# Kernel optimization log

Hardware: AMD Instinct MI355X
Metric: run time of the kernel (lower is better)

## Reference

```python
import jax, jax.numpy as jnp
import numpy as np

D_MODEL = 1024
NUM_HEAD = 16
HEAD_DIM = D_MODEL // NUM_HEAD
D_OUT = 1024
B, S = 2, 2048


def setup_inputs() -> dict:
    key = jax.random.key(0)
    ks = jax.random.split(key, 11)
    s = 0.02
    return {
        "Q": jax.random.normal(ks[0], (B, S, D_MODEL), jnp.float32),
        "K": jax.random.normal(ks[1], (B, S, D_MODEL), jnp.float32),
        "V": jax.random.normal(ks[2], (B, S, D_MODEL), jnp.float32),
        "Wq": jax.random.normal(ks[3], (D_MODEL, D_MODEL), jnp.float32) * s,
        "bq": jnp.zeros((D_MODEL,), jnp.float32),
        "Wk": jax.random.normal(ks[4], (D_MODEL, D_MODEL), jnp.float32) * s,
        "bk": jnp.zeros((D_MODEL,), jnp.float32),
        "Wv": jax.random.normal(ks[5], (D_MODEL, D_MODEL), jnp.float32) * s,
        "bv": jnp.zeros((D_MODEL,), jnp.float32),
        "Wo": jax.random.normal(ks[6], (D_MODEL, D_OUT), jnp.float32) * s,
        "bo": jnp.zeros((D_OUT,), jnp.float32),
    }


def reference(Q, K, V, Wq, bq, Wk, bk, Wv, bv, Wo, bo):
    T = jnp.asarray(HEAD_DIM, Q.dtype) ** 0.5
    b = Q.shape[0]
    q = (Q @ Wq + bq) / T                      # [B,S,D]
    k = K @ Wk + bk
    v = V @ Wv + bv
    q = q.reshape(b, -1, NUM_HEAD, HEAD_DIM)   # [B,S,H,d]
    k = k.reshape(b, -1, NUM_HEAD, HEAD_DIM)
    v = v.reshape(b, -1, NUM_HEAD, HEAD_DIM)
    scores = jnp.einsum("bqhd,bkhd->bhqk", q, k)
    attn = jax.nn.softmax(scores, axis=-1)
    out = jnp.einsum("bhqk,bkhd->bqhd", attn, v).reshape(b, -1, D_MODEL)
    return out @ Wo + bo
```

## Files before the change

kernel.cpp:

```cpp
#include <hip/hip_runtime.h>
#include <cstdint>
#include <cstddef>

#define D_MODEL 1024
#define HD 64
#define NH 16
#define SEQ 2048
#define NB 2

typedef __attribute__((ext_vector_type(8))) short bf8;
typedef __attribute__((ext_vector_type(8))) unsigned short us8;
typedef __attribute__((ext_vector_type(4))) unsigned short us4;
typedef __attribute__((ext_vector_type(4))) float f4;

__device__ __forceinline__ float bf2f(unsigned short u) {
  union { unsigned int i; float f; } c; c.i = ((unsigned int)u) << 16; return c.f;
}
__device__ __forceinline__ unsigned short f2bf(float x) {
  union { float f; unsigned int i; } c; c.f = x;
  unsigned int r = (c.i + 0x7FFFu + ((c.i >> 16) & 1u)) >> 16;
  return (unsigned short)r;
}
__device__ __forceinline__ unsigned int pkbf(float lo, float hi) {
  unsigned int r;
  asm("v_cvt_pk_bf16_f32 %0, %1, %2" : "=v"(r) : "v"(lo), "v"(hi));
  return r;
}
__device__ __forceinline__ float ex2(float x) {
  float r;
  asm("v_exp_f32 %0, %1" : "=v"(r) : "v"(x));
  return r;
}
__device__ __forceinline__ f4 mfma16(bf8 a, bf8 b, f4 c) {
  return __builtin_amdgcn_mfma_f32_16x16x32_bf16(a, b, c, 0, 0, 0);
}
__device__ __forceinline__ void gl16(const unsigned short* g, unsigned short* l) {
  __builtin_amdgcn_global_load_lds(
      (const __attribute__((address_space(1))) unsigned int*)g,
      (__attribute__((address_space(3))) unsigned int*)l, 16, 0, 0);
}

#define QSCALE (0.125f * 1.44269504088896f)

__global__ __launch_bounds__(256) void prep_weights(
    const float* __restrict__ Wq, const float* __restrict__ Wk,
    const float* __restrict__ Wv, const float* __restrict__ Wo,
    unsigned short* __restrict__ wthi) {
  int bid = blockIdx.x;
  int mat = bid >> 10, rem = bid & 1023;
  int kt = (rem >> 5) * 32, nt = (rem & 31) * 32;
  const float* W = (mat == 0) ? Wq : (mat == 1) ? Wk : (mat == 2) ? Wv : Wo;
  unsigned short* oh = wthi + ((size_t)mat << 20);
  __shared__ float ls[32][33];
  int i = threadIdx.x >> 5;
  int jj = threadIdx.x & 31;
#pragma unroll
  for (int ii = 0; ii < 4; ++ii) {
    int r = i + ii * 8;
    ls[r][jj] = W[(size_t)(kt + r) * D_MODEL + nt + jj];
  }
  __syncthreads();
#pragma unroll
  for (int ii = 0; ii < 4; ++ii) {
    int r = i + ii * 8;
    float v = ls[jj][r];
    if (mat == 0) v *= QSCALE;
    oh[(size_t)(nt + r) * D_MODEL + kt + jj] = f2bf(v);
  }
}

__global__ __launch_bounds__(256, 3) void proj_gemm(
    const float* __restrict__ Qin, const float* __restrict__ Kin,
    const float* __restrict__ Vin, const unsigned short* __restrict__ wth,
    const float* __restrict__ b0, const float* __restrict__ b1,
    const float* __restrict__ b2,
    unsigned short* __restrict__ qh, unsigned short* __restrict__ kh,
    unsigned short* __restrict__ vt) {
  int wid = (blockIdx.x & 7) * 96 + (blockIdx.x >> 3);
  int z = wid >> 8, rem = wid & 255, bm = rem >> 3, bn = rem & 7;

  const float* A = (z == 0) ? Qin : (z == 1) ? Kin : Vin;
  const unsigned short* Bh = wth + ((size_t)z << 20);
  const float* bias = (z == 0) ? b0 : (z == 1) ? b1 : b2;
  float bsc = (z == 0) ? QSCALE : 1.0f;

  int tid = threadIdx.x, lane = tid & 63, w = tid >> 6;
  int wr = w >> 1, wc = w & 1, l16 = lane & 15, l4 = lane >> 4;

  __shared__ unsigned short As[2][128 * 32];
  __shared__ unsigned short Bsh[2][128 * 32];

  const float* Ab = A + (size_t)(bm * 128) * D_MODEL;
  const unsigned short* Bhb = Bh + (size_t)(bn * 128) * D_MODEL;

  int r0 = tid >> 2, g0 = tid & 3;
  int r1 = (256 + tid) >> 2, g1 = tid & 3;
  int s0 = (r0 ^ (r0 >> 2)) & 3, s1 = (r1 ^ (r1 >> 2)) & 3;
  size_t so0 = (size_t)r0 * D_MODEL + ((g0 ^ s0) * 8);
  size_t so1 = (size_t)r1 * D_MODEL + ((g1 ^ s1) * 8);
  int ld0 = (w * 64) * 8;
  int ld1 = (256 + w * 64) * 8;

  int rr = tid >> 2, c8 = (tid & 3) * 8;
  int adst[2];
#pragma unroll
  for (int p = 0; p < 2; ++p) {
    int row = p * 64 + rr;
    int sw = (row ^ (row >> 2)) & 3;
    adst[p] = row * 32 + (((tid & 3) ^ sw)) * 8;
  }

  int offA[4], offB[4];
#pragma unroll
  for (int m = 0; m < 4; ++m) {
    int row = wr * 64 + m * 16 + l16;
    int sw = (row ^ (row >> 2)) & 3;
    offA[m] = row * 32 + ((l4 ^ sw)) * 8;
  }
#pragma unroll
  for (int n = 0; n < 4; ++n) {
    int row = wc * 64 + n * 16 + l16;
    int sw = (row ^ (row >> 2)) & 3;
    offB[n] = row * 32 + ((l4 ^ sw)) * 8;
  }

  f4 acc[4][4];
  const f4 zf = {0.f, 0.f, 0.f, 0.f};
#pragma unroll
  for (int m = 0; m < 4; ++m)
#pragma unroll
    for (int n = 0; n < 4; ++n) acc[m][n] = zf;

  {
    float4 x[2][2];
#pragma unroll
    for (int p = 0; p < 2; ++p) {
      const float* src = Ab + (size_t)(p * 64 + rr) * D_MODEL + c8;
      x[p][0] = *reinterpret_cast<const float4*>(src);
      x[p][1] = *reinterpret_cast<const float4*>(src + 4);
    }
    gl16(Bhb + so0, &Bsh[0][ld0]);
    gl16(Bhb + so1, &Bsh[0][ld1]);
#pragma unroll
    for (int p = 0; p < 2; ++p) {
      union { us8 v; unsigned u[4]; } hv;
      hv.u[0] = pkbf(x[p][0].x, x[p][0].y); hv.u[1] = pkbf(x[p][0].z, x[p][0].w);
      hv.u[2] = pkbf(x[p][1].x, x[p][1].y); hv.u[3] = pkbf(x[p][1].z, x[p][1].w);
      *reinterpret_cast<us8*>(&As[0][adst[p]]) = hv.v;
    }
  }
  __syncthreads();

  int cur = 0;
  for (int i = 0; i < 32; ++i) {
    float4 nx[2][2];
    if (i < 31) {
      int ktn = (i + 1) * 32;
#pragma unroll
      for (int p = 0; p < 2; ++p) {
        const float* src = Ab + (size_t)(p * 64 + rr) * D_MODEL + ktn + c8;
        nx[p][0] = *reinterpret_cast<const float4*>(src);
        nx[p][1] = *reinterpret_cast<const float4*>(src + 4);
      }
      gl16(Bhb + ktn + so0, &Bsh[cur ^ 1][ld0]);
      gl16(Bhb + ktn + so1, &Bsh[cur ^ 1][ld1]);
    }
    bf8 a[4], bh[4];
#pragma unroll
    for (int m = 0; m < 4; ++m)
      a[m] = *reinterpret_cast<const bf8*>(&As[cur][offA[m]]);
#pragma unroll
    for (int n = 0; n < 4; ++n)
      bh[n] = *reinterpret_cast<const bf8*>(&Bsh[cur][offB[n]]);
#pragma unroll
    for (int m = 0; m < 4; ++m)
#pragma unroll
      for (int n = 0; n < 4; ++n)
        acc[m][n] = mfma16(a[m], bh[n], acc[m][n]);
    if (i < 31) {
#pragma unroll
      for (int p = 0; p < 2; ++p) {
        union { us8 v; unsigned u[4]; } hv;
        hv.u[0] = pkbf(nx[p][0].x, nx[p][0].y); hv.u[1] = pkbf(nx[p][0].z, nx[p][0].w);
        hv.u[2] = pkbf(nx[p][1].x, nx[p][1].y); hv.u[3] = pkbf(nx[p][1].z, nx[p][1].w);
        *reinterpret_cast<us8*>(&As[cur ^ 1][adst[p]]) = hv.v;
      }
    }
    __syncthreads();
    cur ^= 1;
  }

#pragma unroll
  for (int n = 0; n < 4; ++n) {
    int col = bn * 128 + wc * 64 + n * 16 + l16;
    float bb = bias[col] * bsc;
#pragma unroll
    for (int m = 0; m < 4; ++m) {
      int row0 = bm * 128 + wr * 64 + m * 16 + l4 * 4;
      if (z == 0) {
#pragma unroll
        for (int r = 0; r < 4; ++r)
          qh[(size_t)(row0 + r) * D_MODEL + col] = f2bf(acc[m][n][r] + bb);
      } else if (z == 1) {
#pragma unroll
        for (int r = 0; r < 4; ++r)
          kh[(size_t)(row0 + r) * D_MODEL + col] = f2bf(acc[m][n][r] + bb);
      } else {
        int bb2 = row0 >> 11, ss = row0 & (SEQ - 1);
        int hh2 = col >> 6, dd = col & 63;
        union { us4 s; uint2 u; } pk4;
        pk4.u.x = pkbf(acc[m][n][0] + bb, acc[m][n][1] + bb);
        pk4.u.y = pkbf(acc[m][n][2] + bb, acc[m][n][3] + bb);
        *reinterpret_cast<us4*>(vt + ((size_t)(bb2 * NH + hh2) * HD + dd) * SEQ + ss) = pk4.s;
      }
    }
  }
}

__global__ __launch_bounds__(256, 3) void out_gemm(
    const unsigned short* __restrict__ ah, const unsigned short* __restrict__ wth,
    const float* __restrict__ bo, float* __restrict__ o32) {
  int wid = (blockIdx.x & 7) * 64 + (blockIdx.x >> 3);
  int bm = wid >> 4, bn = wid & 15;

  const unsigned short* Bh = wth + ((size_t)3 << 20);
  int tid = threadIdx.x, lane = tid & 63, w = tid >> 6;
  int wr = w >> 1, wc = w & 1, l16 = lane & 15, l4 = lane >> 4;

  __shared__ unsigned short As[2][128 * 32];
  __shared__ unsigned short Bsh[2][64 * 32];

  const unsigned short* Ab = ah + (size_t)(bm * 128) * D_MODEL;
  const unsigned short* Bhb = Bh + (size_t)(bn * 64) * D_MODEL;

  int r0 = tid >> 2, g0 = tid & 3;
  int r1 = (256 + tid) >> 2;
  int s0 = (r0 ^ (r0 >> 2)) & 3, s1 = (r1 ^ (r1 >> 2)) & 3;
  size_t so0 = (size_t)r0 * D_MODEL + ((g0 ^ s0) * 8);
  size_t so1 = (size_t)r1 * D_MODEL + ((g0 ^ s1) * 8);
  int ld0 = (w * 64) * 8;
  int ld1 = (256 + w * 64) * 8;

  int offA[4], offB[2];
#pragma unroll
  for (int m = 0; m < 4; ++m) {
    int row = wr * 64 + m * 16 + l16;
    int sw = (row ^ (row >> 2)) & 3;
    offA[m] = row * 32 + ((l4 ^ sw)) * 8;
  }
#pragma unroll
  for (int n = 0; n < 2; ++n) {
    int row = wc * 32 + n * 16 + l16;
    int sw = (row ^ (row >> 2)) & 3;
    offB[n] = row * 32 + ((l4 ^ sw)) * 8;
  }

  f4 acc[4][2];
  const f4 zf = {0.f, 0.f, 0.f, 0.f};
#pragma unroll
  for (int m = 0; m < 4; ++m)
#pragma unroll
    for (int n = 0; n < 2; ++n) acc[m][n] = zf;

  gl16(Ab + so0, &As[0][ld0]); gl16(Ab + so1, &As[0][ld1]);
  gl16(Bhb + so0, &Bsh[0][ld0]);
  __syncthreads();

  int cur = 0;
  for (int i = 0; i < 32; ++i) {
    if (i < 31) {
      int ktn = (i + 1) * 32;
      gl16(Ab + ktn + so0, &As[cur ^ 1][ld0]); gl16(Ab + ktn + so1, &As[cur ^ 1][ld1]);
      gl16(Bhb + ktn + so0, &Bsh[cur ^ 1][ld0]);
    }
    bf8 a[4], bh[2];
#pragma unroll
    for (int m = 0; m < 4; ++m)
      a[m] = *reinterpret_cast<const bf8*>(&As[cur][offA[m]]);
#pragma unroll
    for (int n = 0; n < 2; ++n)
      bh[n] = *reinterpret_cast<const bf8*>(&Bsh[cur][offB[n]]);
#pragma unroll
    for (int m = 0; m < 4; ++m)
#pragma unroll
      for (int n = 0; n < 2; ++n)
        acc[m][n] = mfma16(a[m], bh[n], acc[m][n]);
    __syncthreads();
    cur ^= 1;
  }

#pragma unroll
  for (int n = 0; n < 2; ++n) {
    int col = bn * 64 + wc * 32 + n * 16 + l16;
    float bb = bo[col];
#pragma unroll
    for (int m = 0; m < 4; ++m) {
      int row0 = bm * 128 + wr * 64 + m * 16 + l4 * 4;
#pragma unroll
      for (int r = 0; r < 4; ++r)
        o32[(size_t)(row0 + r) * D_MODEL + col] = acc[m][n][r] + bb;
    }
  }
}

__global__ __launch_bounds__(256) void attn_kernel(
    const unsigned short* __restrict__ qh, const unsigned short* __restrict__ kh,
    const unsigned short* __restrict__ vt, unsigned short* __restrict__ aout) {
  int orig = blockIdx.x + (blockIdx.y << 4) + (blockIdx.z << 8);
  int swz = ((orig & 7) << 6) + (orig >> 3);
  int qt = swz & 15, h = (swz >> 4) & 15, b = swz >> 8;

  int tid = threadIdx.x;
  int lane = tid & 63, w = tid >> 6;
  int l16 = lane & 15, l4 = lane >> 4;
  int l8r = lane >> 3, l8c = lane & 7;

  __shared__ unsigned short lds[32768];

  const unsigned short* Kh = kh + (size_t)b * SEQ * D_MODEL + h * HD;
  const unsigned short* Vt = vt + (size_t)(b * NH + h) * HD * SEQ;

  bf8 qf[2][2];
#pragma unroll
  for (int m = 0; m < 2; ++m) {
    size_t qo = (size_t)(b * SEQ + qt * 128 + w * 32 + m * 16 + l16) * D_MODEL + h * HD + l4 * 8;
    qf[m][0] = *reinterpret_cast<const bf8*>(qh + qo);
    qf[m][1] = *reinterpret_cast<const bf8*>(qh + qo + 32);
  }
  bf8 ones;
#pragma unroll
  for (int j = 0; j < 8; ++j) ones[j] = (short)0x3F80;

  const f4 zf = {0.f, 0.f, 0.f, 0.f};
  f4 acc[2][4];
  f4 accs[2] = {zf, zf};
  float mr[2] = {0.f, 0.f};
#pragma unroll
  for (int m = 0; m < 2; ++m)
#pragma unroll
    for (int nt = 0; nt < 4; ++nt) acc[m][nt] = zf;

  const int sgr = (l8c ^ l8r) * 8;
  const int swk = l16 & 7;
  const int vsub = ((l4 & 1) << 2);
  const int vrow_in = lane >> 4;

  {
#pragma unroll
    for (int j = 0; j < 4; ++j) {
      int s = w * 4 + j;
      gl16(Kh + (size_t)(8 * s + l8r) * D_MODEL + sgr, &lds[0 + s * 512]);
      int row = 4 * s + vrow_in;
      int g = ((lane & 7) ^ (row & 7)) | (lane & 8);
      gl16(Vt + (size_t)row * SEQ + g * 8, &lds[16384 + s * 512]);
    }
  }
  __syncthreads();

  int cur = 0;
  for (int kt = 0; kt < SEQ / 128; ++kt) {
    if (kt < SEQ / 128 - 1) {
      int k0n = (kt + 1) * 128;
      unsigned short* kd = &lds[(cur ^ 1) * 8192];
      unsigned short* vd = &lds[16384 + (cur ^ 1) * 8192];
#pragma unroll
      for (int j = 0; j < 4; ++j) {
        int s = w * 4 + j;
        gl16(Kh + (size_t)(k0n + 8 * s + l8r) * D_MODEL + sgr, kd + s * 512);
        int row = 4 * s + vrow_in;
        int g = ((lane & 7) ^ (row & 7)) | (lane & 8);
        gl16(Vt + (size_t)row * SEQ + k0n + g * 8, vd + s * 512);
      }
    }
    const unsigned short* khb = &lds[cur * 8192];
    const unsigned short* vlb = &lds[16384 + cur * 8192];

#pragma unroll
    for (int h2 = 0; h2 < 2; ++h2) {
      const unsigned short* khh = khb + h2 * 4096;
      bf8 kb[4][2];
#pragma unroll
      for (int c = 0; c < 4; ++c) {
        int row = c * 16 + l16;
        kb[c][0] = *reinterpret_cast<const bf8*>(&khh[row * 64 + ((l4 ^ swk) * 8)]);
        kb[c][1] = *reinterpret_cast<const bf8*>(&khh[row * 64 + (((4 + l4) ^ swk) * 8)]);
      }
      f4 sc[2][4];
      __builtin_amdgcn_s_setprio(1);
#pragma unroll
      for (int m = 0; m < 2; ++m)
#pragma unroll
        for (int c = 0; c < 4; ++c) {
          f4 sv = zf;
          sv = mfma16(kb[c][0], qf[m][0], sv);
          sv = mfma16(kb[c][1], qf[m][1], sv);
          sc[m][c] = sv;
        }
      __builtin_amdgcn_s_setprio(0);
      uint2 vdr[4][4];
#pragma unroll
      for (int c = 0; c < 4; ++c) {
        int gvc = 2 * c + (l4 >> 1);
        int voff = (((gvc ^ swk) + 8 * h2) << 3) + vsub;
#pragma unroll
        for (int nt = 0; nt < 4; ++nt)
          vdr[c][nt] = *reinterpret_cast<const uint2*>(&vlb[(nt * 16 + l16) * 128 + voff]);
      }
      unsigned Wp[2][4][2];
#pragma unroll
      for (int m = 0; m < 2; ++m) {
        float tc0 = fmaxf(fmaxf(sc[m][0][0], sc[m][0][1]), fmaxf(sc[m][0][2], sc[m][0][3]));
        float tc1 = fmaxf(fmaxf(sc[m][1][0], sc[m][1][1]), fmaxf(sc[m][1][2], sc[m][1][3]));
        float tc2 = fmaxf(fmaxf(sc[m][2][0], sc[m][2][1]), fmaxf(sc[m][2][2], sc[m][2][3]));
        float tc3 = fmaxf(fmaxf(sc[m][3][0], sc[m][3][1]), fmaxf(sc[m][3][2], sc[m][3][3]));
        float tm = fmaxf(fmaxf(tc0, tc1), fmaxf(tc2, tc3));
        tm = fmaxf(tm, __shfl_xor(tm, 16));
        tm = fmaxf(tm, __shfl_xor(tm, 32));
        if (__any(tm > mr[m] + 8.0f)) {
          float mn = fmaxf(mr[m], tm);
          float al = ex2(mr[m] - mn);
          mr[m] = mn;
          accs[m][0] *= al; accs[m][1] *= al; accs[m][2] *= al; accs[m][3] *= al;
#pragma unroll
          for (int nt = 0; nt < 4; ++nt) {
            acc[m][nt][0] *= al; acc[m][nt][1] *= al;
            acc[m][nt][2] *= al; acc[m][nt][3] *= al;
          }
        }
#pragma unroll
        for (int c = 0; c < 4; ++c) {
          float p0 = ex2(sc[m][c][0] - mr[m]);
          float p1 = ex2(sc[m][c][1] - mr[m]);
          float p2 = ex2(sc[m][c][2] - mr[m]);
          float p3 = ex2(sc[m][c][3] - mr[m]);
          Wp[m][c][0] = pkbf(p0, p1);
          Wp[m][c][1] = pkbf(p2, p3);
        }
      }
      __builtin_amdgcn_s_setprio(1);
#pragma unroll
      for (int cp = 0; cp < 2; ++cp) {
        int c0 = cp * 2, c1 = cp * 2 + 1;
#pragma unroll
        for (int m = 0; m < 2; ++m) {
          union { bf8 v; unsigned u[4]; } pu;
          pu.u[0] = Wp[m][c0][0]; pu.u[1] = Wp[m][c0][1];
          pu.u[2] = Wp[m][c1][0]; pu.u[3] = Wp[m][c1][1];
          accs[m] = mfma16(ones, pu.v, accs[m]);
#pragma unroll
          for (int nt = 0; nt < 4; ++nt) {
            union { bf8 v; unsigned u[4]; } vu;
            vu.u[0] = vdr[c0][nt].x; vu.u[1] = vdr[c0][nt].y;
            vu.u[2] = vdr[c1][nt].x; vu.u[3] = vdr[c1][nt].y;
            acc[m][nt] = mfma16(vu.v, pu.v, acc[m][nt]);
          }
        }
      }
      __builtin_amdgcn_s_setprio(0);
    }
    __syncthreads();
    cur ^= 1;
  }

  float inv[2];
#pragma unroll
  for (int m = 0; m < 2; ++m) inv[m] = 1.0f / accs[m][0];
#pragma unroll
  for (int m = 0; m < 2; ++m) {
    int q = w * 32 + m * 16 + l16;
    int sw = (q & 7) << 3;
#pragma unroll
    for (int nt = 0; nt < 4; ++nt) {
      uint2 pw;
      pw.x = pkbf(acc[m][nt][0] * inv[m], acc[m][nt][1] * inv[m]);
      pw.y = pkbf(acc[m][nt][2] * inv[m], acc[m][nt][3] * inv[m]);
      int d0 = nt * 16 + l4 * 4;
      *reinterpret_cast<uint2*>(&lds[q * 64 + (d0 ^ sw)]) = pw;
    }
  }
  __syncthreads();
  {
    int q = tid >> 1, dh = (tid & 1) * 32, sw = (q & 7) << 3;
    size_t orow = ((size_t)(b * SEQ + qt * 128 + q)) * D_MODEL + h * HD + dh;
#pragma unroll
    for (int j = 0; j < 4; ++j) {
      us8 vv = *reinterpret_cast<const us8*>(&lds[q * 64 + ((dh + j * 8) ^ sw)]);
      *reinterpret_cast<us8*>(&aout[orow + j * 8]) = vv;
    }
  }
}

extern "C" void kernel_launch(void* const* d_in, const int* in_sizes, int n_in,
                              void* d_out, int out_size, void* d_ws, size_t ws_size,
                              hipStream_t stream) {
  const float* Q  = (const float*)d_in[0];
  const float* K  = (const float*)d_in[1];
  const float* V  = (const float*)d_in[2];
  const float* Wq = (const float*)d_in[3];
  const float* bq = (const float*)d_in[4];
  const float* Wk = (const float*)d_in[5];
  const float* bk = (const float*)d_in[6];
  const float* Wv = (const float*)d_in[7];
  const float* bv = (const float*)d_in[8];
  const float* Wo = (const float*)d_in[9];
  const float* bo = (const float*)d_in[10];
  float* out = (float*)d_out;

  unsigned char* ws = (unsigned char*)d_ws;
  const size_t MB = 1024 * 1024;
  unsigned short* wthi = (unsigned short*)(ws);
  unsigned short* qh   = (unsigned short*)(ws + 8 * MB);
  unsigned short* kh   = (unsigned short*)(ws + 16 * MB);
  unsigned short* vt   = (unsigned short*)(ws + 24 * MB);
  unsigned short* ah   = (unsigned short*)(ws + 32 * MB);

  prep_weights<<<dim3(4096, 1, 1), 256, 0, stream>>>(Wq, Wk, Wv, Wo, wthi);
  proj_gemm<<<dim3(768, 1, 1), 256, 0, stream>>>(Q, K, V, wthi,
                                                 bq, bk, bv, qh, kh, vt);
  attn_kernel<<<dim3(16, NH, NB), 256, 0, stream>>>(qh, kh, vt, ah);
  out_gemm<<<dim3(512, 1, 1), 256, 0, stream>>>(ah, wthi, bo, out);
}
```

Baseline: 128.5 us.

## Double attention query tile to 256 rows per block to reuse K/V loads

Each attention block now handles 256 query rows (64 per wave, four 16-row m-tiles) instead of 128. The K and V fragments loaded from LDS are reused across twice as many query rows, which halves the global and LDS traffic for K/V per query. The m-tiles are processed in two groups so the score registers stay bounded. In exchange the grid shrinks to 256 blocks on a 256-CU-class GPU and register pressure rises (launch_bounds min 1 block), which can hurt latency hiding.

```diff
diff --git a/kernel.cpp b/kernel.cpp
--- a/kernel.cpp
+++ b/kernel.cpp
@@ -303,12 +303,12 @@
   }
 }
 
-__global__ __launch_bounds__(256) void attn_kernel(
+__global__ __launch_bounds__(256, 1) void attn_kernel(
     const unsigned short* __restrict__ qh, const unsigned short* __restrict__ kh,
     const unsigned short* __restrict__ vt, unsigned short* __restrict__ aout) {
-  int orig = blockIdx.x + (blockIdx.y << 4) + (blockIdx.z << 8);
-  int swz = ((orig & 7) << 6) + (orig >> 3);
-  int qt = swz & 15, h = (swz >> 4) & 15, b = swz >> 8;
+  int orig = blockIdx.x + (blockIdx.y << 3) + (blockIdx.z << 7);
+  int swz = ((orig & 7) << 5) + (orig >> 3);
+  int qt = swz & 7, h = (swz >> 3) & 15, b = swz >> 7;
 
   int tid = threadIdx.x;
   int lane = tid & 63, w = tid >> 6;
@@ -320,10 +320,10 @@
   const unsigned short* Kh = kh + (size_t)b * SEQ * D_MODEL + h * HD;
   const unsigned short* Vt = vt + (size_t)(b * NH + h) * HD * SEQ;
 
-  bf8 qf[2][2];
-#pragma unroll
-  for (int m = 0; m < 2; ++m) {
-    size_t qo = (size_t)(b * SEQ + qt * 128 + w * 32 + m * 16 + l16) * D_MODEL + h * HD + l4 * 8;
+  bf8 qf[4][2];
+#pragma unroll
+  for (int m = 0; m < 4; ++m) {
+    size_t qo = (size_t)(b * SEQ + qt * 256 + w * 64 + m * 16 + l16) * D_MODEL + h * HD + l4 * 8;
     qf[m][0] = *reinterpret_cast<const bf8*>(qh + qo);
     qf[m][1] = *reinterpret_cast<const bf8*>(qh + qo + 32);
   }
@@ -332,11 +332,11 @@
   for (int j = 0; j < 8; ++j) ones[j] = (short)0x3F80;
 
   const f4 zf = {0.f, 0.f, 0.f, 0.f};
-  f4 acc[2][4];
-  f4 accs[2] = {zf, zf};
-  float mr[2] = {0.f, 0.f};
-#pragma unroll
-  for (int m = 0; m < 2; ++m)
+  f4 acc[4][4];
+  f4 accs[4] = {zf, zf, zf, zf};
+  float mr[4] = {0.f, 0.f, 0.f, 0.f};
+#pragma unroll
+  for (int m = 0; m < 4; ++m)
 #pragma unroll
     for (int nt = 0; nt < 4; ++nt) acc[m][nt] = zf;
 
@@ -385,18 +385,6 @@
         kb[c][0] = *reinterpret_cast<const bf8*>(&khh[row * 64 + ((l4 ^ swk) * 8)]);
         kb[c][1] = *reinterpret_cast<const bf8*>(&khh[row * 64 + (((4 + l4) ^ swk) * 8)]);
       }
-      f4 sc[2][4];
-      __builtin_amdgcn_s_setprio(1);
-#pragma unroll
-      for (int m = 0; m < 2; ++m)
-#pragma unroll
-        for (int c = 0; c < 4; ++c) {
-          f4 sv = zf;
-          sv = mfma16(kb[c][0], qf[m][0], sv);
-          sv = mfma16(kb[c][1], qf[m][1], sv);
-          sc[m][c] = sv;
-        }
-      __builtin_amdgcn_s_setprio(0);
       uint2 vdr[4][4];
 #pragma unroll
       for (int c = 0; c < 4; ++c) {
@@ -406,68 +394,85 @@
         for (int nt = 0; nt < 4; ++nt)
           vdr[c][nt] = *reinterpret_cast<const uint2*>(&vlb[(nt * 16 + l16) * 128 + voff]);
       }
-      unsigned Wp[2][4][2];
-#pragma unroll
-      for (int m = 0; m < 2; ++m) {
-        float tc0 = fmaxf(fmaxf(sc[m][0][0], sc[m][0][1]), fmaxf(sc[m][0][2], sc[m][0][3]));
-        float tc1 = fmaxf(fmaxf(sc[m][1][0], sc[m][1][1]), fmaxf(sc[m][1][2], sc[m][1][3]));
-        float tc2 = fmaxf(fmaxf(sc[m][2][0], sc[m][2][1]), fmaxf(sc[m][2][2], sc[m][2][3]));
-        float tc3 = fmaxf(fmaxf(sc[m][3][0], sc[m][3][1]), fmaxf(sc[m][3][2], sc[m][3][3]));
-        float tm = fmaxf(fmaxf(tc0, tc1), fmaxf(tc2, tc3));
-        tm = fmaxf(tm, __shfl_xor(tm, 16));
-        tm = fmaxf(tm, __shfl_xor(tm, 32));
-        if (__any(tm > mr[m] + 8.0f)) {
-          float mn = fmaxf(mr[m], tm);
-          float al = ex2(mr[m] - mn);
-          mr[m] = mn;
-          accs[m][0] *= al; accs[m][1] *= al; accs[m][2] *= al; accs[m][3] *= al;
-#pragma unroll
-          for (int nt = 0; nt < 4; ++nt) {
-            acc[m][nt][0] *= al; acc[m][nt][1] *= al;
-            acc[m][nt][2] *= al; acc[m][nt][3] *= al;
+#pragma unroll
+      for (int mg = 0; mg < 2; ++mg) {
+        f4 sc[2][4];
+        __builtin_amdgcn_s_setprio(1);
+#pragma unroll
+        for (int mi = 0; mi < 2; ++mi)
+#pragma unroll
+          for (int c = 0; c < 4; ++c) {
+            f4 sv = zf;
+            sv = mfma16(kb[c][0], qf[mg * 2 + mi][0], sv);
+            sv = mfma16(kb[c][1], qf[mg * 2 + mi][1], sv);
+            sc[mi][c] = sv;
+          }
+        __builtin_amdgcn_s_setprio(0);
+        unsigned Wp[2][4][2];
+#pragma unroll
+        for (int mi = 0; mi < 2; ++mi) {
+          int m = mg * 2 + mi;
+          float tc0 = fmaxf(fmaxf(sc[mi][0][0], sc[mi][0][1]), fmaxf(sc[mi][0][2], sc[mi][0][3]));
+          float tc1 = fmaxf(fmaxf(sc[mi][1][0], sc[mi][1][1]), fmaxf(sc[mi][1][2], sc[mi][1][3]));
+          float tc2 = fmaxf(fmaxf(sc[mi][2][0], sc[mi][2][1]), fmaxf(sc[mi][2][2], sc[mi][2][3]));
+          float tc3 = fmaxf(fmaxf(sc[mi][3][0], sc[mi][3][1]), fmaxf(sc[mi][3][2], sc[mi][3][3]));
+          float tm = fmaxf(fmaxf(tc0, tc1), fmaxf(tc2, tc3));
+          tm = fmaxf(tm, __shfl_xor(tm, 16));
+          tm = fmaxf(tm, __shfl_xor(tm, 32));
+          if (__any(tm > mr[m] + 8.0f)) {
+            float mn = fmaxf(mr[m], tm);
+            float al = ex2(mr[m] - mn);
+            mr[m] = mn;
+            accs[m][0] *= al; accs[m][1] *= al; accs[m][2] *= al; accs[m][3] *= al;
+#pragma unroll
+            for (int nt = 0; nt < 4; ++nt) {
+              acc[m][nt][0] *= al; acc[m][nt][1] *= al;
+              acc[m][nt][2] *= al; acc[m][nt][3] *= al;
+            }
+          }
+#pragma unroll
+          for (int c = 0; c < 4; ++c) {
+            float p0 = ex2(sc[mi][c][0] - mr[m]);
+            float p1 = ex2(sc[mi][c][1] - mr[m]);
+            float p2 = ex2(sc[mi][c][2] - mr[m]);
+            float p3 = ex2(sc[mi][c][3] - mr[m]);
+            Wp[mi][c][0] = pkbf(p0, p1);
+            Wp[mi][c][1] = pkbf(p2, p3);
           }
         }
-#pragma unroll
-        for (int c = 0; c < 4; ++c) {
-          float p0 = ex2(sc[m][c][0] - mr[m]);
-          float p1 = ex2(sc[m][c][1] - mr[m]);
-          float p2 = ex2(sc[m][c][2] - mr[m]);
-          float p3 = ex2(sc[m][c][3] - mr[m]);
-          Wp[m][c][0] = pkbf(p0, p1);
-          Wp[m][c][1] = pkbf(p2, p3);
-        }
-      }
-      __builtin_amdgcn_s_setprio(1);
-#pragma unroll
-      for (int cp = 0; cp < 2; ++cp) {
-        int c0 = cp * 2, c1 = cp * 2 + 1;
-#pragma unroll
-        for (int m = 0; m < 2; ++m) {
-          union { bf8 v; unsigned u[4]; } pu;
-          pu.u[0] = Wp[m][c0][0]; pu.u[1] = Wp[m][c0][1];
-          pu.u[2] = Wp[m][c1][0]; pu.u[3] = Wp[m][c1][1];
-          accs[m] = mfma16(ones, pu.v, accs[m]);
-#pragma unroll
-          for (int nt = 0; nt < 4; ++nt) {
-            union { bf8 v; unsigned u[4]; } vu;
-            vu.u[0] = vdr[c0][nt].x; vu.u[1] = vdr[c0][nt].y;
-            vu.u[2] = vdr[c1][nt].x; vu.u[3] = vdr[c1][nt].y;
-            acc[m][nt] = mfma16(vu.v, pu.v, acc[m][nt]);
+        __builtin_amdgcn_s_setprio(1);
+#pragma unroll
+        for (int cp = 0; cp < 2; ++cp) {
+          int c0 = cp * 2, c1 = cp * 2 + 1;
+#pragma unroll
+          for (int mi = 0; mi < 2; ++mi) {
+            int m = mg * 2 + mi;
+            union { bf8 v; unsigned u[4]; } pu;
+            pu.u[0] = Wp[mi][c0][0]; pu.u[1] = Wp[mi][c0][1];
+            pu.u[2] = Wp[mi][c1][0]; pu.u[3] = Wp[mi][c1][1];
+            accs[m] = mfma16(ones, pu.v, accs[m]);
+#pragma unroll
+            for (int nt = 0; nt < 4; ++nt) {
+              union { bf8 v; unsigned u[4]; } vu;
+              vu.u[0] = vdr[c0][nt].x; vu.u[1] = vdr[c0][nt].y;
+              vu.u[2] = vdr[c1][nt].x; vu.u[3] = vdr[c1][nt].y;
+              acc[m][nt] = mfma16(vu.v, pu.v, acc[m][nt]);
+            }
           }
         }
-      }
-      __builtin_amdgcn_s_setprio(0);
+        __builtin_amdgcn_s_setprio(0);
+      }
     }
     __syncthreads();
     cur ^= 1;
   }
 
-  float inv[2];
-#pragma unroll
-  for (int m = 0; m < 2; ++m) inv[m] = 1.0f / accs[m][0];
-#pragma unroll
-  for (int m = 0; m < 2; ++m) {
-    int q = w * 32 + m * 16 + l16;
+  float inv[4];
+#pragma unroll
+  for (int m = 0; m < 4; ++m) inv[m] = 1.0f / accs[m][0];
+#pragma unroll
+  for (int m = 0; m < 4; ++m) {
+    int q = w * 64 + m * 16 + l16;
     int sw = (q & 7) << 3;
 #pragma unroll
     for (int nt = 0; nt < 4; ++nt) {
@@ -479,9 +484,10 @@
     }
   }
   __syncthreads();
-  {
-    int q = tid >> 1, dh = (tid & 1) * 32, sw = (q & 7) << 3;
-    size_t orow = ((size_t)(b * SEQ + qt * 128 + q)) * D_MODEL + h * HD + dh;
+#pragma unroll
+  for (int rr2 = 0; rr2 < 2; ++rr2) {
+    int q = rr2 * 128 + (tid >> 1), dh = (tid & 1) * 32, sw = (q & 7) << 3;
+    size_t orow = ((size_t)(b * SEQ + qt * 256 + q)) * D_MODEL + h * HD + dh;
 #pragma unroll
     for (int j = 0; j < 4; ++j) {
       us8 vv = *reinterpret_cast<const us8*>(&lds[q * 64 + ((dh + j * 8) ^ sw)]);
@@ -517,6 +523,6 @@
   prep_weights<<<dim3(4096, 1, 1), 256, 0, stream>>>(Wq, Wk, Wv, Wo, wthi);
   proj_gemm<<<dim3(768, 1, 1), 256, 0, stream>>>(Q, K, V, wthi,
                                                  bq, bk, bv, qh, kh, vt);
-  attn_kernel<<<dim3(16, NH, NB), 256, 0, stream>>>(qh, kh, vt, ah);
+  attn_kernel<<<dim3(8, NH, NB), 256, 0, stream>>>(qh, kh, vt, ah);
   out_gemm<<<dim3(512, 1, 1), 256, 0, stream>>>(ah, wthi, bo, out);
 }
```

Measured after the change: 145.4 us. +13.1%, slower.
